# Performance work log

Hardware: AMD Instinct MI355X
Metric: run time of the kernel (lower is better)

## Reference

```python
import jax, jax.numpy as jnp
import numpy as np

WS = 8          # window size
NH = 16         # num heads
C = 256         # in_channels
L = WS * WS     # tokens per window
EPS = 1e-5      # LayerNorm eps

def _rel_index():
    coords = np.stack(np.meshgrid(np.arange(WS), np.arange(WS), indexing='ij')).reshape(2, -1)
    rel = coords[:, :, None] - coords[:, None, :]
    rel = rel + (WS - 1)
    rel[0] = rel[0] * (2 * WS - 1)
    return jnp.asarray(rel.sum(0))  # [L, L] int

REL_IDX = _rel_index()

def _ln(x, g, b):
    m = x.mean(-1, keepdims=True)
    v = jnp.var(x, axis=-1, keepdims=True)
    return (x - m) * jax.lax.rsqrt(v + EPS) * g + b

def setup_inputs() -> dict:
    key = jax.random.key(0)
    ks = jax.random.split(key, 8)
    return {
        'x': jax.random.normal(ks[0], (2, C, 256, 256), dtype=jnp.float32),
        'pre_gamma': jnp.ones((C,), jnp.float32),
        'pre_beta': jnp.zeros((C,), jnp.float32),
        'post_gamma': jnp.ones((C,), jnp.float32),
        'post_beta': jnp.zeros((C,), jnp.float32),
        'qkv_w': jax.random.normal(ks[1], (C, 3 * C), jnp.float32) * 0.02,
        'qkv_b': jnp.zeros((3 * C,), jnp.float32),
        'proj_w': jax.random.normal(ks[2], (C, C), jnp.float32) * 0.02,
        'proj_b': jnp.zeros((C,), jnp.float32),
        'rel_bias_table': jax.random.normal(ks[3], ((2 * WS - 1) ** 2, NH), jnp.float32) * 0.02,
    }

def reference(x, pre_gamma, pre_beta, post_gamma, post_beta, qkv_w, qkv_b, proj_w, proj_b, rel_bias_table):
    N, Cc, H, W = x.shape
    # block partition: [N,C,H,W] -> [N*nWin, L, C]
    t = x.reshape(N, Cc, H // WS, WS, W // WS, WS)
    t = t.transpose(0, 2, 4, 3, 5, 1).reshape(-1, L, Cc)
    B = t.shape[0]
    # pre-norm + relative self-attention (cosine / normalized qk)
    y = _ln(t, pre_gamma, pre_beta)
    qkv = (y @ qkv_w + qkv_b).reshape(B, L, 3, NH, Cc // NH).transpose(2, 0, 3, 1, 4)
    q, k, v = qkv[0], qkv[1], qkv[2]  # [B, h, L, dh]
    q = q / jnp.maximum(jnp.linalg.norm(q, axis=-1, keepdims=True), 1e-12)
    k = k / jnp.maximum(jnp.linalg.norm(k, axis=-1, keepdims=True), 1e-12)
    bias = rel_bias_table[REL_IDX].transpose(2, 0, 1)  # [h, L, L]
    attn = jax.nn.softmax(jnp.einsum('bhld,bhmd->bhlm', q, k) + bias, axis=-1)
    o = jnp.einsum('bhlm,bhmd->bhld', attn, v).transpose(0, 2, 1, 3).reshape(B, L, Cc)
    o = o @ proj_w + proj_b
    out = t + o
    # post-norm residual (mlp is Identity in MetNet-3)
    out = out + _ln(out, post_gamma, post_beta)
    # reverse partition -> [N, C, H, W]
    out = out.reshape(N, H // WS, W // WS, WS, WS, Cc)
    out = out.transpose(0, 5, 1, 3, 2, 4).reshape(N, Cc, H, W)
    return out
```

## Files before the change

### kernel.cpp

```cpp
#include <hip/hip_runtime.h>


#define WSZ 8
#define LTOK 64
#define NH 16
#define CCH 256
#define WW2 256
#define HWP 65536
#define NWIN 2048

#define TP 258
#define QP2 18
#define VP2 66
#define PP2 66
#define OHP 36

typedef __bf16 bf16x8 __attribute__((ext_vector_type(8)));
typedef float  f32x4  __attribute__((ext_vector_type(4)));
typedef unsigned short u16;
typedef uint4  __attribute__((may_alias)) uint4_a;
typedef float4 __attribute__((may_alias)) float4_a;

__device__ __forceinline__ float b2f(u16 u) {
    return (float)__builtin_bit_cast(__bf16, u);
}
__device__ __forceinline__ u16 f2b(float f) {
    return __builtin_bit_cast(u16, (__bf16)f);
}
__device__ __forceinline__ __bf16 u2b(u16 u) {
    return __builtin_bit_cast(__bf16, u);
}
__device__ __forceinline__ float gload(const void* p, int idx, int isf32) {
    return isf32 ? ((const float*)p)[idx] : b2f(((const u16*)p)[idx]);
}

static __global__ void detect_dtype(const u16* __restrict__ xu, int* __restrict__ flag) {
    int lane = threadIdx.x;
    u16 u = xu[lane];
    int e = (u >> 7) & 0xFF;
    bool plaus = (u == 0) || (e >= 0x6C && e <= 0x86);
    unsigned long long m = __ballot(plaus);
    if (lane == 0) flag[0] = (__popcll(m) >= 56) ? 0 : 1;
}

static __global__ __launch_bounds__(256) void prep_qkv(
        const void* __restrict__ qkv_w, const void* __restrict__ qkv_b,
        const void* __restrict__ g, const void* __restrict__ be,
        u16* __restrict__ gwT, float* __restrict__ D2, float* __restrict__ D3,
        const int* __restrict__ flagp)
{
    const int isf32 = flagp[0];
    int col = blockIdx.x;
    int c   = threadIdx.x;
    float gv = gload(g, c, isf32), bv = gload(be, c, isf32);
    float wv = gload(qkv_w, c * 768 + col, isf32);
    gwT[col * 256 + c] = f2b(gv * wv);
    float s2 = gv * wv, s3 = bv * wv;
    #pragma unroll
    for (int off = 32; off; off >>= 1) {
        s2 += __shfl_xor(s2, off);
        s3 += __shfl_xor(s3, off);
    }
    __shared__ float p2[4], p3[4];
    int wvid = threadIdx.x >> 6, ln = threadIdx.x & 63;
    if (ln == 0) { p2[wvid] = s2; p3[wvid] = s3; }
    __syncthreads();
    if (threadIdx.x == 0) {
        D2[col] = p2[0] + p2[1] + p2[2] + p2[3];
        D3[col] = p3[0] + p3[1] + p3[2] + p3[3] + gload(qkv_b, col, isf32);
    }
}

static __global__ __launch_bounds__(256) void prep_proj(
        const void* __restrict__ proj_w, u16* __restrict__ pwT,
        const void* __restrict__ table, float* __restrict__ tablef,
        const int* __restrict__ flagp)
{
    const int isf32 = flagp[0];
    int nrow = blockIdx.x, k = threadIdx.x;
    pwT[nrow * 256 + k] = f2b(gload(proj_w, k * 256 + nrow, isf32));
    int gid = blockIdx.x * 256 + threadIdx.x;
    if (gid < (2 * WSZ - 1) * (2 * WSZ - 1) * NH)
        tablef[gid] = gload(table, gid, isf32);
}

static __global__ __launch_bounds__(256, 2) void win_attn(
    const void* __restrict__ x, void* __restrict__ out,
    const u16* __restrict__ gwT, const u16* __restrict__ pwT,
    const float* __restrict__ D2, const float* __restrict__ D3,
    const void* __restrict__ proj_b, const void* __restrict__ postg,
    const void* __restrict__ postb, const float* __restrict__ tablef,
    const int* __restrict__ flagp)
{
    __shared__ u16 sm_t[LTOK * TP];
    __shared__ u16 sm_q[4][LTOK * QP2];
    __shared__ u16 sm_k[4][LTOK * QP2];
    __shared__ u16 sm_vt[4][NH * VP2];
    __shared__ u16 sm_p[LTOK * PP2];
    __shared__ u16 sm_oh[LTOK * OHP];
    __shared__ float sm_mean[LTOK], sm_rstd[LTOK];
    __shared__ u16 sm_zero[16];

    const int isf32 = flagp[0];
    const int tid  = threadIdx.x;
    const int wv   = tid >> 6;
    const int lane = tid & 63;
    const int quad = lane >> 4;
    const int n15  = lane & 15;

    const int b  = blockIdx.x;
    const int nb = b >> 10, wh = (b >> 5) & 31, wwi = b & 31;
    const int base = nb * (CCH * HWP) + wh * (8 * WW2) + wwi * 8;

    if (tid < 16) sm_zero[tid] = 0;

    if (isf32) {
        const float* xf = (const float*)x;
        #pragma unroll
        for (int r = 0; r < 8; ++r) {
            int s = tid + r * 256;
            int c = s >> 3, i = s & 7;
            const float* src = xf + base + c * HWP + i * WW2;
            float4 a = *(const float4_a*)(src);
            float4 d = *(const float4_a*)(src + 4);
            u16* dst = &sm_t[(i * 8) * TP + c];
            dst[0 * TP] = f2b(a.x);  dst[1 * TP] = f2b(a.y);
            dst[2 * TP] = f2b(a.z);  dst[3 * TP] = f2b(a.w);
            dst[4 * TP] = f2b(d.x);  dst[5 * TP] = f2b(d.y);
            dst[6 * TP] = f2b(d.z);  dst[7 * TP] = f2b(d.w);
        }
    } else {
        const u16* xu = (const u16*)x;
        #pragma unroll
        for (int r = 0; r < 8; ++r) {
            int s = tid + r * 256;
            int c = s >> 3, i = s & 7;
            const uint4 v = *(const uint4_a*)(xu + base + c * HWP + i * WW2);
            u16* dst = &sm_t[(i * 8) * TP + c];
            dst[0 * TP] = (u16)(v.x & 0xffff);  dst[1 * TP] = (u16)(v.x >> 16);
            dst[2 * TP] = (u16)(v.y & 0xffff);  dst[3 * TP] = (u16)(v.y >> 16);
            dst[4 * TP] = (u16)(v.z & 0xffff);  dst[5 * TP] = (u16)(v.z >> 16);
            dst[6 * TP] = (u16)(v.w & 0xffff);  dst[7 * TP] = (u16)(v.w >> 16);
        }
    }
    __syncthreads();

    {
        int l = tid >> 2, g = tid & 3;
        float s = 0.f, ss = 0.f;
        const u16* row = &sm_t[l * TP + g * 64];
        #pragma unroll
        for (int e = 0; e < 64; ++e) {
            float a = b2f(row[e]);
            s += a; ss += a * a;
        }
        s += __shfl_xor(s, 1); ss += __shfl_xor(ss, 1);
        s += __shfl_xor(s, 2); ss += __shfl_xor(ss, 2);
        if (g == 0) {
            float mean = s * (1.f / 256.f);
            float var  = ss * (1.f / 256.f) - mean * mean;
            sm_mean[l] = mean;
            sm_rstd[l] = rsqrtf(var + 1e-5f);
        }
    }

    float s4[4], ms4[4];
    #pragma unroll
    for (int r = 0; r < 4; ++r) {
        int tok = wv * 16 + quad * 4 + r;
        float mu = sm_mean[tok], sd = sm_rstd[tok];
        s4[r] = sd; ms4[r] = -mu * sd;
    }

    bf16x8 afr[8];
    {
        const u16* arow = &sm_t[(wv * 16 + n15) * TP];
        #pragma unroll
        for (int kb = 0; kb < 8; ++kb) {
            #pragma unroll
            for (int j = 0; j < 8; ++j)
                afr[kb][j] = u2b(arow[kb * 32 + quad * 8 + j]);
        }
    }

    int toff[4][4];
    #pragma unroll
    for (int ct = 0; ct < 4; ++ct) {
        int key = ct * 16 + n15, im = key >> 3, jm = key & 7;
        #pragma unroll
        for (int r = 0; r < 4; ++r) {
            int tok = wv * 16 + quad * 4 + r;
            int il = tok >> 3, jl = tok & 7;
            toff[ct][r] = ((il - im + 7) * 15 + (jl - jm + 7)) * 16;
        }
    }

    f32x4 accp[16];
    #pragma unroll
    for (int t2 = 0; t2 < 16; ++t2) accp[t2] = f32x4{0.f, 0.f, 0.f, 0.f};
    const f32x4 zero4 = f32x4{0.f, 0.f, 0.f, 0.f};

    bf16x8 onesf;
    #pragma unroll
    for (int j = 0; j < 8; ++j) onesf[j] = (__bf16)1.0f;

    for (int hq = 0; hq < 4; ++hq) {
        const int H = hq * 4;

        f32x4 aq[4], ak[4], av[4];
        #pragma unroll
        for (int hh = 0; hh < 4; ++hh) { aq[hh] = zero4; ak[hh] = zero4; av[hh] = zero4; }
        const u16* g0 = &gwT[(H * 16 + n15) * 256 + quad * 8];
        #pragma unroll
        for (int kb = 0; kb < 8; ++kb) {
            #pragma unroll
            for (int hh = 0; hh < 4; ++hh) {
                const u16* gq = g0 + hh * 4096 + kb * 32;
                bf16x8 bq = __builtin_bit_cast(bf16x8, *(const uint4_a*)(gq));
                bf16x8 bk = __builtin_bit_cast(bf16x8, *(const uint4_a*)(gq + 65536));
                bf16x8 bv = __builtin_bit_cast(bf16x8, *(const uint4_a*)(gq + 131072));
                aq[hh] = __builtin_amdgcn_mfma_f32_16x16x32_bf16(afr[kb], bq, aq[hh], 0, 0, 0);
                ak[hh] = __builtin_amdgcn_mfma_f32_16x16x32_bf16(afr[kb], bk, ak[hh], 0, 0, 0);
                av[hh] = __builtin_amdgcn_mfma_f32_16x16x32_bf16(afr[kb], bv, av[hh], 0, 0, 0);
            }
        }
        #pragma unroll
        for (int hh = 0; hh < 4; ++hh) {
            int ci = (H + hh) * 16 + n15;
            float d2q = D2[ci],       d3q = D3[ci];
            float d2k = D2[256 + ci], d3k = D3[256 + ci];
            float d2v = D2[512 + ci], d3v = D3[512 + ci];
            float qv[4], kv[4], vv[4];
            #pragma unroll
            for (int r = 0; r < 4; ++r) {
                qv[r] = s4[r] * aq[hh][r] + ms4[r] * d2q + d3q;
                kv[r] = s4[r] * ak[hh][r] + ms4[r] * d2k + d3k;
                vv[r] = s4[r] * av[hh][r] + ms4[r] * d2v + d3v;
            }
            #pragma unroll
            for (int r = 0; r < 4; ++r) {
                float sq = qv[r] * qv[r], sk = kv[r] * kv[r];
                sq += __shfl_xor(sq, 1); sk += __shfl_xor(sk, 1);
                sq += __shfl_xor(sq, 2); sk += __shfl_xor(sk, 2);
                sq += __shfl_xor(sq, 4); sk += __shfl_xor(sk, 4);
                sq += __shfl_xor(sq, 8); sk += __shfl_xor(sk, 8);
                qv[r] *= rsqrtf(fmaxf(sq, 1e-24f));
                kv[r] *= rsqrtf(fmaxf(sk, 1e-24f));
            }
            #pragma unroll
            for (int r = 0; r < 4; ++r) {
                int tok = wv * 16 + quad * 4 + r;
                sm_q[hh][tok * QP2 + n15] = f2b(qv[r]);
                sm_k[hh][tok * QP2 + n15] = f2b(kv[r]);
                sm_vt[hh][n15 * VP2 + tok] = f2b(vv[r]);
            }
        }
        __syncthreads();

        #pragma unroll
        for (int hh = 0; hh < 4; ++hh) {
            const int h = H + hh;
            f32x4 sc[4];
            {
                bf16x8 aqf;
                const u16* qrow = (quad < 2) ? &sm_q[hh][(wv * 16 + n15) * QP2 + quad * 8]
                                             : sm_zero;
                #pragma unroll
                for (int j = 0; j < 8; ++j) aqf[j] = u2b(qrow[j]);
                #pragma unroll
                for (int ct = 0; ct < 4; ++ct) {
                    bf16x8 bkf;
                    const u16* krow = (quad < 2) ? &sm_k[hh][(ct * 16 + n15) * QP2 + quad * 8]
                                                 : sm_zero;
                    #pragma unroll
                    for (int j = 0; j < 8; ++j) bkf[j] = u2b(krow[j]);
                    f32x4 bias;
                    #pragma unroll
                    for (int r = 0; r < 4; ++r) bias[r] = tablef[toff[ct][r] + h];
                    sc[ct] = __builtin_amdgcn_mfma_f32_16x16x32_bf16(aqf, bkf, bias, 0, 0, 0);
                }
            }
            #pragma unroll
            for (int r = 0; r < 4; ++r) {
                float e0 = __expf(sc[0][r]), e1 = __expf(sc[1][r]);
                float e2 = __expf(sc[2][r]), e3 = __expf(sc[3][r]);
                int tok = wv * 16 + quad * 4 + r;
                sm_p[tok * PP2 +  0 + n15] = f2b(e0);
                sm_p[tok * PP2 + 16 + n15] = f2b(e1);
                sm_p[tok * PP2 + 32 + n15] = f2b(e2);
                sm_p[tok * PP2 + 48 + n15] = f2b(e3);
            }

            f32x4 ov = zero4, rs = zero4;
            #pragma unroll
            for (int ks = 0; ks < 2; ++ks) {
                bf16x8 ap, bvf;
                const u16* prow = &sm_p[(wv * 16 + n15) * PP2 + ks * 32 + quad * 8];
                const u16* vrow = &sm_vt[hh][n15 * VP2 + ks * 32 + quad * 8];
                #pragma unroll
                for (int j = 0; j < 8; ++j) { ap[j] = u2b(prow[j]); bvf[j] = u2b(vrow[j]); }
                ov = __builtin_amdgcn_mfma_f32_16x16x32_bf16(ap, bvf, ov, 0, 0, 0);
                rs = __builtin_amdgcn_mfma_f32_16x16x32_bf16(ap, onesf, rs, 0, 0, 0);
            }
            #pragma unroll
            for (int r = 0; r < 4; ++r) {
                int tok = wv * 16 + quad * 4 + r;
                sm_oh[tok * OHP + (h & 1) * 16 + n15] = f2b(ov[r] / rs[r]);
            }

            if (hh & 1) {
                int hp = h >> 1;
                bf16x8 aof;
                const u16* orow = &sm_oh[(wv * 16 + n15) * OHP + quad * 8];
                #pragma unroll
                for (int j = 0; j < 8; ++j) aof[j] = u2b(orow[j]);
                const u16* pwb = &pwT[n15 * 256 + hp * 32 + quad * 8];
                #pragma unroll
                for (int t2 = 0; t2 < 16; ++t2) {
                    bf16x8 bpf = __builtin_bit_cast(bf16x8, *(const uint4_a*)(pwb + t2 * 16 * 256));
                    accp[t2] = __builtin_amdgcn_mfma_f32_16x16x32_bf16(aof, bpf, accp[t2], 0, 0, 0);
                }
            }
        }
        __syncthreads();
    }

    {
        #pragma unroll
        for (int t2 = 0; t2 < 16; ++t2) {
            int col = t2 * 16 + n15;
            float pb = gload(proj_b, col, isf32);
            #pragma unroll
            for (int r = 0; r < 4; ++r) {
                int tok = wv * 16 + quad * 4 + r;
                accp[t2][r] += pb + b2f(sm_t[tok * TP + col]);
            }
        }
        float sr[4] = {0, 0, 0, 0}, ssr[4] = {0, 0, 0, 0};
        #pragma unroll
        for (int t2 = 0; t2 < 16; ++t2) {
            #pragma unroll
            for (int r = 0; r < 4; ++r) { float v = accp[t2][r]; sr[r] += v; ssr[r] += v * v; }
        }
        #pragma unroll
        for (int r = 0; r < 4; ++r) {
            sr[r] += __shfl_xor(sr[r], 1); ssr[r] += __shfl_xor(ssr[r], 1);
            sr[r] += __shfl_xor(sr[r], 2); ssr[r] += __shfl_xor(ssr[r], 2);
            sr[r] += __shfl_xor(sr[r], 4); ssr[r] += __shfl_xor(ssr[r], 4);
            sr[r] += __shfl_xor(sr[r], 8); ssr[r] += __shfl_xor(ssr[r], 8);
        }
        float mean2[4], rs2[4];
        #pragma unroll
        for (int r = 0; r < 4; ++r) {
            float m = sr[r] * (1.f / 256.f);
            float v = ssr[r] * (1.f / 256.f) - m * m;
            mean2[r] = m; rs2[r] = rsqrtf(v + 1e-5f);
        }
        #pragma unroll
        for (int t2 = 0; t2 < 16; ++t2) {
            int col = t2 * 16 + n15;
            float pg = gload(postg, col, isf32), pb2 = gload(postb, col, isf32);
            #pragma unroll
            for (int r = 0; r < 4; ++r) {
                int tok = wv * 16 + quad * 4 + r;
                float o1 = accp[t2][r];
                float fin = o1 + (o1 - mean2[r]) * rs2[r] * pg + pb2;
                sm_t[tok * TP + col] = f2b(fin);
            }
        }
    }
    __syncthreads();

    if (isf32) {
        float* outf = (float*)out;
        #pragma unroll
        for (int r = 0; r < 8; ++r) {
            int s = tid + r * 256;
            int c = s >> 3, i = s & 7;
            const u16* src = &sm_t[(i * 8) * TP + c];
            float* dst = outf + base + c * HWP + i * WW2;
            float4 a, d;
            a.x = b2f(src[0 * TP]); a.y = b2f(src[1 * TP]);
            a.z = b2f(src[2 * TP]); a.w = b2f(src[3 * TP]);
            d.x = b2f(src[4 * TP]); d.y = b2f(src[5 * TP]);
            d.z = b2f(src[6 * TP]); d.w = b2f(src[7 * TP]);
            *(float4_a*)dst = a;
            *(float4_a*)(dst + 4) = d;
        }
    } else {
        u16* outu = (u16*)out;
        #pragma unroll
        for (int r = 0; r < 8; ++r) {
            int s = tid + r * 256;
            int c = s >> 3, i = s & 7;
            const u16* src = &sm_t[(i * 8) * TP + c];
            uint4 v;
            v.x = (unsigned)src[0 * TP] | ((unsigned)src[1 * TP] << 16);
            v.y = (unsigned)src[2 * TP] | ((unsigned)src[3 * TP] << 16);
            v.z = (unsigned)src[4 * TP] | ((unsigned)src[5 * TP] << 16);
            v.w = (unsigned)src[6 * TP] | ((unsigned)src[7 * TP] << 16);
            *(uint4_a*)(outu + base + c * HWP + i * WW2) = v;
        }
    }
}

extern "C" void kernel_launch(void* const* d_in, const int* in_sizes, int n_in,
                              void* d_out, int out_size, void* d_ws, size_t ws_size,
                              hipStream_t stream) {
    const void* x     = d_in[0];
    const void* preg  = d_in[1];
    const void* preb  = d_in[2];
    const void* postg = d_in[3];
    const void* postb = d_in[4];
    const void* qkvw  = d_in[5];
    const void* qkvb  = d_in[6];
    const void* projw = d_in[7];
    const void* projb = d_in[8];
    const void* table = d_in[9];

    char* ws = (char*)d_ws;
    u16*   gwT = (u16*)(ws);
    u16*   pwT = (u16*)(ws + 393216);
    float* D2  = (float*)(ws + 524288);
    float* D3  = (float*)(ws + 527360);
    float* tbf = (float*)(ws + 530432);
    int*   flg = (int*)(ws + 544832);

    detect_dtype<<<1, 64, 0, stream>>>((const u16*)x, flg);
    prep_qkv<<<768, 256, 0, stream>>>(qkvw, qkvb, preg, preb, gwT, D2, D3, flg);
    prep_proj<<<256, 256, 0, stream>>>(projw, pwT, table, tbf, flg);
    win_attn<<<NWIN, 256, 0, stream>>>(x, d_out, gwT, pwT, D2, D3,
                                       projb, postg, postb, tbf, flg);
}
```

Measured before the change: 976.3 us.

## Alias shared-memory buffers and reload the input tile to double occupancy

The attention kernel's separate LDS arrays are packed into one buffer, with the q/k/v/p/o scratch overlapping the input-tile region. The input window is then re-read from global memory after attention to rebuild the residual. This cuts per-block LDS from about 73KB to about 40KB, so the launch bound can ask for 4 blocks per CU instead of 2 to better hide latency. The cost is a second global read of x and tighter register limits, which could cause spills given the large accumulator and fragment arrays. The prep kernels are also vectorized to handle four columns per thread.

```diff
diff --git a/kernel.cpp b/kernel.cpp
--- a/kernel.cpp
+++ b/kernel.cpp
@@ -18,8 +18,10 @@
 typedef __bf16 bf16x8 __attribute__((ext_vector_type(8)));
 typedef float  f32x4  __attribute__((ext_vector_type(4)));
 typedef unsigned short u16;
+typedef unsigned long long ull;
 typedef uint4  __attribute__((may_alias)) uint4_a;
 typedef float4 __attribute__((may_alias)) float4_a;
+typedef ull    __attribute__((may_alias)) ull_a;
 
 __device__ __forceinline__ float b2f(u16 u) {
     return (float)__builtin_bit_cast(__bf16, u);
@@ -50,24 +52,45 @@
         const int* __restrict__ flagp)
 {
     const int isf32 = flagp[0];
-    int col = blockIdx.x;
-    int c   = threadIdx.x;
+    int col0 = blockIdx.x * 4;
+    int c    = threadIdx.x;
     float gv = gload(g, c, isf32), bv = gload(be, c, isf32);
-    float wv = gload(qkv_w, c * 768 + col, isf32);
-    gwT[col * 256 + c] = f2b(gv * wv);
-    float s2 = gv * wv, s3 = bv * wv;
+    float w4[4];
+    if (isf32) {
+        float4 w = *(const float4_a*)((const float*)qkv_w + c * 768 + col0);
+        w4[0] = w.x; w4[1] = w.y; w4[2] = w.z; w4[3] = w.w;
+    } else {
+        ull u = *(const ull_a*)((const u16*)qkv_w + c * 768 + col0);
+        w4[0] = b2f((u16)u);         w4[1] = b2f((u16)(u >> 16));
+        w4[2] = b2f((u16)(u >> 32)); w4[3] = b2f((u16)(u >> 48));
+    }
+    float s2[4], s3[4];
+    #pragma unroll
+    for (int j = 0; j < 4; ++j) {
+        float gw = gv * w4[j];
+        gwT[(col0 + j) * 256 + c] = f2b(gw);
+        s2[j] = gw; s3[j] = bv * w4[j];
+    }
     #pragma unroll
     for (int off = 32; off; off >>= 1) {
-        s2 += __shfl_xor(s2, off);
-        s3 += __shfl_xor(s3, off);
-    }
-    __shared__ float p2[4], p3[4];
+        #pragma unroll
+        for (int j = 0; j < 4; ++j) {
+            s2[j] += __shfl_xor(s2[j], off);
+            s3[j] += __shfl_xor(s3[j], off);
+        }
+    }
+    __shared__ float p2[4][4], p3[4][4];
     int wvid = threadIdx.x >> 6, ln = threadIdx.x & 63;
-    if (ln == 0) { p2[wvid] = s2; p3[wvid] = s3; }
+    if (ln == 0) {
+        #pragma unroll
+        for (int j = 0; j < 4; ++j) { p2[wvid][j] = s2[j]; p3[wvid][j] = s3[j]; }
+    }
     __syncthreads();
-    if (threadIdx.x == 0) {
-        D2[col] = p2[0] + p2[1] + p2[2] + p2[3];
-        D3[col] = p3[0] + p3[1] + p3[2] + p3[3] + gload(qkv_b, col, isf32);
+    if (threadIdx.x < 4) {
+        int j = threadIdx.x;
+        D2[col0 + j] = p2[0][j] + p2[1][j] + p2[2][j] + p2[3][j];
+        D3[col0 + j] = p3[0][j] + p3[1][j] + p3[2][j] + p3[3][j]
+                     + gload(qkv_b, col0 + j, isf32);
     }
 }
 
@@ -77,14 +100,24 @@
         const int* __restrict__ flagp)
 {
     const int isf32 = flagp[0];
-    int nrow = blockIdx.x, k = threadIdx.x;
-    pwT[nrow * 256 + k] = f2b(gload(proj_w, k * 256 + nrow, isf32));
+    int n0 = blockIdx.x * 4, k = threadIdx.x;
+    float w4[4];
+    if (isf32) {
+        float4 w = *(const float4_a*)((const float*)proj_w + k * 256 + n0);
+        w4[0] = w.x; w4[1] = w.y; w4[2] = w.z; w4[3] = w.w;
+    } else {
+        ull u = *(const ull_a*)((const u16*)proj_w + k * 256 + n0);
+        w4[0] = b2f((u16)u);         w4[1] = b2f((u16)(u >> 16));
+        w4[2] = b2f((u16)(u >> 32)); w4[3] = b2f((u16)(u >> 48));
+    }
+    #pragma unroll
+    for (int j = 0; j < 4; ++j) pwT[(n0 + j) * 256 + k] = f2b(w4[j]);
     int gid = blockIdx.x * 256 + threadIdx.x;
     if (gid < (2 * WSZ - 1) * (2 * WSZ - 1) * NH)
         tablef[gid] = gload(table, gid, isf32);
 }
 
-static __global__ __launch_bounds__(256, 2) void win_attn(
+static __global__ __launch_bounds__(256, 4) void win_attn(
     const void* __restrict__ x, void* __restrict__ out,
     const u16* __restrict__ gwT, const u16* __restrict__ pwT,
     const float* __restrict__ D2, const float* __restrict__ D3,
@@ -92,12 +125,13 @@
     const void* __restrict__ postb, const float* __restrict__ tablef,
     const int* __restrict__ flagp)
 {
-    __shared__ u16 sm_t[LTOK * TP];
-    __shared__ u16 sm_q[4][LTOK * QP2];
-    __shared__ u16 sm_k[4][LTOK * QP2];
-    __shared__ u16 sm_vt[4][NH * VP2];
-    __shared__ u16 sm_p[LTOK * PP2];
-    __shared__ u16 sm_oh[LTOK * OHP];
+    __shared__ __align__(16) u16 smu[19968];
+    u16* const sm_t  = smu;
+    u16* const sm_qb = smu;
+    u16* const sm_kb = smu + 4608;
+    u16* const sm_vb = smu + 9216;
+    u16* const sm_pb = smu + 13440;
+    u16* const sm_ob = smu + 17664;
     __shared__ float sm_mean[LTOK], sm_rstd[LTOK];
     __shared__ u16 sm_zero[16];
 
@@ -182,6 +216,7 @@
                 afr[kb][j] = u2b(arow[kb * 32 + quad * 8 + j]);
         }
     }
+    __syncthreads();
 
     int toff[4][4];
     #pragma unroll
@@ -250,9 +285,9 @@
             #pragma unroll
             for (int r = 0; r < 4; ++r) {
                 int tok = wv * 16 + quad * 4 + r;
-                sm_q[hh][tok * QP2 + n15] = f2b(qv[r]);
-                sm_k[hh][tok * QP2 + n15] = f2b(kv[r]);
-                sm_vt[hh][n15 * VP2 + tok] = f2b(vv[r]);
+                sm_qb[hh * 1152 + tok * QP2 + n15] = f2b(qv[r]);
+                sm_kb[hh * 1152 + tok * QP2 + n15] = f2b(kv[r]);
+                sm_vb[hh * 1056 + n15 * VP2 + tok] = f2b(vv[r]);
             }
         }
         __syncthreads();
@@ -263,15 +298,17 @@
             f32x4 sc[4];
             {
                 bf16x8 aqf;
-                const u16* qrow = (quad < 2) ? &sm_q[hh][(wv * 16 + n15) * QP2 + quad * 8]
-                                             : sm_zero;
+                const u16* qrow = (quad < 2)
+                    ? &sm_qb[hh * 1152 + (wv * 16 + n15) * QP2 + quad * 8]
+                    : sm_zero;
                 #pragma unroll
                 for (int j = 0; j < 8; ++j) aqf[j] = u2b(qrow[j]);
                 #pragma unroll
                 for (int ct = 0; ct < 4; ++ct) {
                     bf16x8 bkf;
-                    const u16* krow = (quad < 2) ? &sm_k[hh][(ct * 16 + n15) * QP2 + quad * 8]
-                                                 : sm_zero;
+                    const u16* krow = (quad < 2)
+                        ? &sm_kb[hh * 1152 + (ct * 16 + n15) * QP2 + quad * 8]
+                        : sm_zero;
                     #pragma unroll
                     for (int j = 0; j < 8; ++j) bkf[j] = u2b(krow[j]);
                     f32x4 bias;
@@ -285,18 +322,18 @@
                 float e0 = __expf(sc[0][r]), e1 = __expf(sc[1][r]);
                 float e2 = __expf(sc[2][r]), e3 = __expf(sc[3][r]);
                 int tok = wv * 16 + quad * 4 + r;
-                sm_p[tok * PP2 +  0 + n15] = f2b(e0);
-                sm_p[tok * PP2 + 16 + n15] = f2b(e1);
-                sm_p[tok * PP2 + 32 + n15] = f2b(e2);
-                sm_p[tok * PP2 + 48 + n15] = f2b(e3);
+                sm_pb[tok * PP2 +  0 + n15] = f2b(e0);
+                sm_pb[tok * PP2 + 16 + n15] = f2b(e1);
+                sm_pb[tok * PP2 + 32 + n15] = f2b(e2);
+                sm_pb[tok * PP2 + 48 + n15] = f2b(e3);
             }
 
             f32x4 ov = zero4, rs = zero4;
             #pragma unroll
             for (int ks = 0; ks < 2; ++ks) {
                 bf16x8 ap, bvf;
-                const u16* prow = &sm_p[(wv * 16 + n15) * PP2 + ks * 32 + quad * 8];
-                const u16* vrow = &sm_vt[hh][n15 * VP2 + ks * 32 + quad * 8];
+                const u16* prow = &sm_pb[(wv * 16 + n15) * PP2 + ks * 32 + quad * 8];
+                const u16* vrow = &sm_vb[hh * 1056 + n15 * VP2 + ks * 32 + quad * 8];
                 #pragma unroll
                 for (int j = 0; j < 8; ++j) { ap[j] = u2b(prow[j]); bvf[j] = u2b(vrow[j]); }
                 ov = __builtin_amdgcn_mfma_f32_16x16x32_bf16(ap, bvf, ov, 0, 0, 0);
@@ -305,13 +342,13 @@
             #pragma unroll
             for (int r = 0; r < 4; ++r) {
                 int tok = wv * 16 + quad * 4 + r;
-                sm_oh[tok * OHP + (h & 1) * 16 + n15] = f2b(ov[r] / rs[r]);
+                sm_ob[tok * OHP + (h & 1) * 16 + n15] = f2b(ov[r] / rs[r]);
             }
 
             if (hh & 1) {
                 int hp = h >> 1;
                 bf16x8 aof;
-                const u16* orow = &sm_oh[(wv * 16 + n15) * OHP + quad * 8];
+                const u16* orow = &sm_ob[(wv * 16 + n15) * OHP + quad * 8];
                 #pragma unroll
                 for (int j = 0; j < 8; ++j) aof[j] = u2b(orow[j]);
                 const u16* pwb = &pwT[n15 * 256 + hp * 32 + quad * 8];
@@ -324,6 +361,37 @@
         }
         __syncthreads();
     }
+
+    if (isf32) {
+        const float* xf = (const float*)x;
+        #pragma unroll
+        for (int r = 0; r < 8; ++r) {
+            int s = tid + r * 256;
+            int c = s >> 3, i = s & 7;
+            const float* src = xf + base + c * HWP + i * WW2;
+            float4 a = *(const float4_a*)(src);
+            float4 d = *(const float4_a*)(src + 4);
+            u16* dst = &sm_t[(i * 8) * TP + c];
+            dst[0 * TP] = f2b(a.x);  dst[1 * TP] = f2b(a.y);
+            dst[2 * TP] = f2b(a.z);  dst[3 * TP] = f2b(a.w);
+            dst[4 * TP] = f2b(d.x);  dst[5 * TP] = f2b(d.y);
+            dst[6 * TP] = f2b(d.z);  dst[7 * TP] = f2b(d.w);
+        }
+    } else {
+        const u16* xu = (const u16*)x;
+        #pragma unroll
+        for (int r = 0; r < 8; ++r) {
+            int s = tid + r * 256;
+            int c = s >> 3, i = s & 7;
+            const uint4 v = *(const uint4_a*)(xu + base + c * HWP + i * WW2);
+            u16* dst = &sm_t[(i * 8) * TP + c];
+            dst[0 * TP] = (u16)(v.x & 0xffff);  dst[1 * TP] = (u16)(v.x >> 16);
+            dst[2 * TP] = (u16)(v.y & 0xffff);  dst[3 * TP] = (u16)(v.y >> 16);
+            dst[4 * TP] = (u16)(v.z & 0xffff);  dst[5 * TP] = (u16)(v.z >> 16);
+            dst[6 * TP] = (u16)(v.w & 0xffff);  dst[7 * TP] = (u16)(v.w >> 16);
+        }
+    }
+    __syncthreads();
 
     {
         #pragma unroll
@@ -427,8 +495,8 @@
     int*   flg = (int*)(ws + 544832);
 
     detect_dtype<<<1, 64, 0, stream>>>((const u16*)x, flg);
-    prep_qkv<<<768, 256, 0, stream>>>(qkvw, qkvb, preg, preb, gwT, D2, D3, flg);
-    prep_proj<<<256, 256, 0, stream>>>(projw, pwT, table, tbf, flg);
+    prep_qkv<<<192, 256, 0, stream>>>(qkvw, qkvb, preg, preb, gwT, D2, D3, flg);
+    prep_proj<<<64, 256, 0, stream>>>(projw, pwT, table, tbf, flg);
     win_attn<<<NWIN, 256, 0, stream>>>(x, d_out, gwT, pwT, D2, D3,
                                        projb, postg, postb, tbf, flg);
 }
```

Measured after the change: 1.201 ms. 1.23x slower.
